# Kernel optimization log

Hardware: AMD Instinct MI355X
Metric: run time of the kernel (lower is better)

## Reference

```python
import jax, jax.numpy as jnp
import numpy as np

C = 512
GROUPS = 32
EPS = 1e-6


def setup_inputs() -> dict:
    key = jax.random.key(0)
    ks = jax.random.split(key, 10)
    s = 0.02
    return {
        "x": jax.random.normal(ks[0], (2, C, 64, 64), dtype=jnp.float32),
        "gn_scale": jnp.ones((C,), jnp.float32),
        "gn_bias": jnp.zeros((C,), jnp.float32),
        "wq": jax.random.normal(ks[1], (C, C), jnp.float32) * s,
        "bq": jnp.zeros((C,), jnp.float32),
        "wk": jax.random.normal(ks[2], (C, C), jnp.float32) * s,
        "bk": jnp.zeros((C,), jnp.float32),
        "wv": jax.random.normal(ks[3], (C, C), jnp.float32) * s,
        "bv": jnp.zeros((C,), jnp.float32),
        "wo": jax.random.normal(ks[4], (C, C), jnp.float32) * s,
        "bo": jnp.zeros((C,), jnp.float32),
    }


def group_norm(x, scale, bias):
    # x: [b, c, h, w]; 32 groups over channel dim
    b, c, h, w = x.shape
    xg = x.reshape(b, GROUPS, c // GROUPS, h, w)
    mean = jnp.mean(xg, axis=(2, 3, 4), keepdims=True)
    var = jnp.var(xg, axis=(2, 3, 4), keepdims=True)
    xg = (xg - mean) * jax.lax.rsqrt(var + EPS)
    x = xg.reshape(b, c, h, w)
    return x * scale[None, :, None, None] + bias[None, :, None, None]


def reference(x, gn_scale, gn_bias, wq, bq, wk, bk, wv, bv, wo, bo):
    b, c, h, w = x.shape
    n = h * w
    hn = group_norm(x, gn_scale, gn_bias).reshape(b, c, n)  # [b,c,n]
    # 1x1 conv == channel matmul: out[b,o,n] = W[o,i] @ h[b,i,n] + bias
    q = jnp.einsum('oi,bin->bon', wq, hn) + bq[None, :, None]
    k = jnp.einsum('oi,bin->bon', wk, hn) + bk[None, :, None]
    v = jnp.einsum('oi,bin->bon', wv, hn) + bv[None, :, None]
    # weight[b, i, j] = q_i . k_j, softmax over j
    scale = int(c) ** (-0.5)
    weight = jnp.einsum('bci,bcj->bij', q, k) * scale  # [b,n,n]
    weight = jax.nn.softmax(weight, axis=2)
    # h[b,c,i] = sum_j v[b,c,j] * weight[b,i,j]
    out = jnp.einsum('bcj,bij->bci', v, weight)
    out = jnp.einsum('oi,bin->bon', wo, out) + bo[None, :, None]
    return out.reshape(b, c, h, w) + x
```

## Files before the change

### kernel.cpp

```cpp
#include <hip/hip_runtime.h>
#include <hip/hip_bf16.h>


typedef __attribute__((ext_vector_type(8))) short short8_t;
typedef __attribute__((ext_vector_type(4))) short short4_t;
typedef __attribute__((ext_vector_type(4))) float f32x4;

__device__ __forceinline__ void gload16(const void* g, void* l) {
  __builtin_amdgcn_global_load_lds(
      (const __attribute__((address_space(1))) void*)g,
      (__attribute__((address_space(3))) void*)l, 16, 0, 0);
}

__device__ __forceinline__ short f2bf_bits(float f) {
  __hip_bfloat16 h = __float2bfloat16(f);
  return *reinterpret_cast<short*>(&h);
}
__device__ __forceinline__ float bfbits2f(short s) {
  union { unsigned int u; float f; } c;
  c.u = ((unsigned int)(unsigned short)s) << 16;
  return c.f;
}

__global__ __launch_bounds__(512)
void s_gemm8(const __hip_bfloat16* __restrict__ qk,
             __hip_bfloat16* __restrict__ P, float c)
{
  const long long QKz = 4096LL * 1024;
  const long long SS  = 4096LL * 4096;

  const int b = blockIdx.x;
  const int bz = b >> 8;
  const int r = b & 255, xcd = r & 7, sl = r >> 3;
  const int bm = (xcd >> 1) * 4 + (sl & 3);
  const int bn = (xcd & 1) * 8 + (sl >> 2);

  const __hip_bfloat16* Aq = qk + (size_t)bz * QKz;
  const __hip_bfloat16* Bk = Aq + 512;

  const int tid = threadIdx.x;
  const int wid = tid >> 6, l = tid & 63;
  const int wrM = wid >> 2, wcN = wid & 3;
  const int lhi = l >> 4, llo = l & 15;

  __shared__ char sm[2 * 65536];

  f32x4 acc[2][2][4][2] = {};
  short8_t af[4][2], bf[2][2];

  const int rIn = l >> 3;
  const int colSw = 8 * ((l & 7) ^ (rIn & 7));
  const __hip_bfloat16* gA = Aq + (size_t)(bm * 256 + rIn) * 1024 + colSw;
  const __hip_bfloat16* gB = Bk + (size_t)(bn * 256 + rIn) * 1024 + colSw;

  auto STG = [&](int mat, int half, int t) {
    const __hip_bfloat16* src = mat ? gB : gA;
    char* dst = sm + (t & 1) * 65536 + mat * 32768;
    const int rb = half * 128 + wid * 16;
    gload16(src + (size_t)rb * 1024 + t * 64, dst + rb * 128);
    gload16(src + (size_t)(rb + 8) * 1024 + t * 64, dst + (rb + 8) * 128);
  };

#define PHASE(MH, NH, RBUF, WAITN, LA, LB, ...) do {                          \
    asm volatile("s_waitcnt vmcnt(" #WAITN ")" ::: "memory");                 \
    __builtin_amdgcn_sched_barrier(0);                                        \
    const char* bbA = sm + (RBUF) * 65536;                                    \
    const char* bbB = bbA + 32768;                                            \
    if (LA) {                                                                 \
      _Pragma("unroll") for (int m = 0; m < 4; ++m) {                         \
        const int rowA = (MH) * 128 + wrM * 64 + m * 16 + llo;                \
        _Pragma("unroll") for (int kk = 0; kk < 2; ++kk)                      \
          af[m][kk] = *(const short8_t*)(bbA + rowA * 128 +                   \
                        (((kk * 4 + lhi) ^ (rowA & 7)) * 16));                \
      }                                                                       \
    }                                                                         \
    if (LB) {                                                                 \
      _Pragma("unroll") for (int n = 0; n < 2; ++n) {                         \
        const int rowB = (NH) * 128 + wcN * 32 + n * 16 + llo;                \
        _Pragma("unroll") for (int kk = 0; kk < 2; ++kk)                      \
          bf[n][kk] = *(const short8_t*)(bbB + rowB * 128 +                   \
                        (((kk * 4 + lhi) ^ (rowB & 7)) * 16));                \
      }                                                                       \
    }                                                                         \
    __VA_ARGS__;                                                              \
    __builtin_amdgcn_sched_barrier(0);                                        \
    __builtin_amdgcn_s_barrier();                                             \
    __builtin_amdgcn_sched_barrier(0);                                        \
    __builtin_amdgcn_s_setprio(1);                                            \
    _Pragma("unroll") for (int kk = 0; kk < 2; ++kk)                          \
      _Pragma("unroll") for (int m = 0; m < 4; ++m)                           \
        _Pragma("unroll") for (int n = 0; n < 2; ++n)                         \
          acc[MH][NH][m][n] = __builtin_amdgcn_mfma_f32_16x16x32_bf16(        \
              af[m][kk], bf[n][kk], acc[MH][NH][m][n], 0, 0, 0);              \
    __builtin_amdgcn_s_setprio(0);                                            \
    __builtin_amdgcn_sched_barrier(0);                                        \
    __builtin_amdgcn_s_barrier();                                             \
    __builtin_amdgcn_sched_barrier(0);                                        \
  } while (0)

  STG(0, 0, 0); STG(1, 0, 0); STG(0, 1, 0); STG(1, 1, 0);
  STG(0, 0, 1); STG(1, 0, 1); STG(0, 1, 1); STG(1, 1, 1);
  asm volatile("s_waitcnt vmcnt(0)" ::: "memory");
  __builtin_amdgcn_sched_barrier(0);
  __builtin_amdgcn_s_barrier();
  __builtin_amdgcn_sched_barrier(0);

  for (int i = 0; i < 3; ++i) {
    const int t1 = 2 * i + 1, t2 = 2 * i + 2, t3 = 2 * i + 3;
    PHASE(0, 0, 0, 4, 1, 1, if (i >= 1) STG(1, 0, t1));
    PHASE(0, 1, 0, 4, 0, 1, STG(0, 0, t2));
    PHASE(1, 1, 0, 4, 1, 0, STG(1, 1, t2));
    PHASE(1, 0, 0, 4, 0, 1, STG(0, 1, t2));
    PHASE(0, 0, 1, 4, 1, 1, STG(1, 0, t2));
    PHASE(0, 1, 1, 4, 0, 1, STG(0, 0, t3));
    PHASE(1, 1, 1, 4, 1, 0, STG(1, 1, t3));
    PHASE(1, 0, 1, 4, 0, 1, STG(0, 1, t3));
  }
  {
    PHASE(0, 0, 0, 0, 1, 1, STG(1, 0, 7));
    PHASE(0, 1, 0, 0, 0, 1, );
    PHASE(1, 1, 0, 0, 1, 0, );
    PHASE(1, 0, 0, 0, 0, 1, );
    PHASE(0, 0, 1, 0, 1, 1, );
    PHASE(0, 1, 1, 0, 0, 1, );
    PHASE(1, 1, 1, 0, 1, 0, );
    PHASE(1, 0, 1, 0, 0, 1, );
  }
#undef PHASE

  __hip_bfloat16* Pb = P + (size_t)bz * SS;
#pragma unroll
  for (int Mh = 0; Mh < 2; ++Mh)
#pragma unroll
    for (int m = 0; m < 4; ++m)
#pragma unroll
      for (int rr = 0; rr < 4; ++rr) {
        const int grow = bm * 256 + Mh * 128 + wrM * 64 + m * 16 + lhi * 4 + rr;
#pragma unroll
        for (int Nh = 0; Nh < 2; ++Nh)
#pragma unroll
          for (int n = 0; n < 2; ++n) {
            const int gcol = bn * 256 + Nh * 128 + wcN * 32 + n * 16 + llo;
            Pb[(size_t)grow * 4096 + gcol] =
                __float2bfloat16(exp2f(acc[Mh][Nh][m][n][rr] * c));
          }
      }
}

__global__ __launch_bounds__(256)
void rowsum_recip(const __hip_bfloat16* __restrict__ P, float* __restrict__ rs,
                  long long strZ)
{
  const int row = blockIdx.x, z = blockIdx.y;
  const __hip_bfloat16* p = P + (size_t)z * strZ + (size_t)row * 4096;
  const int tid = threadIdx.x;
  short8_t a = *(const short8_t*)(p + tid * 16);
  short8_t bq = *(const short8_t*)(p + tid * 16 + 8);
  float s = 0.f;
#pragma unroll
  for (int i = 0; i < 8; ++i) { s += bfbits2f(a[i]); s += bfbits2f(bq[i]); }
#pragma unroll
  for (int o = 32; o; o >>= 1) s += __shfl_xor(s, o);
  __shared__ float red[4];
  if ((tid & 63) == 0) red[tid >> 6] = s;
  __syncthreads();
  if (tid == 0) {
    s = red[0] + red[1] + red[2] + red[3];
    rs[(size_t)z * 4096 + row] = 1.f / s;
  }
}

template<int OUTF, int BIASMODE, int RESID, int PIPE, int SWZ, int MF, int NORM>
__global__ __launch_bounds__(256, 2)
void gemm_nt(const __hip_bfloat16* __restrict__ A,
             const __hip_bfloat16* __restrict__ B,
             void* __restrict__ Cv,
             const float* __restrict__ bias,
             const float* __restrict__ resid,
             const float* __restrict__ rnorm,
             float scale, int M, int N, int K,
             int lda, int ldb, int ldc,
             long long strA, long long strB, long long strC, long long strR)
{
  int bm, bn, bz;
  if (SWZ == 0) {
    bm = blockIdx.x; bn = blockIdx.y; bz = blockIdx.z;
  } else if (SWZ == 2) {
    const int b = blockIdx.x;
    bz = b >> 10;
    const int b2 = b & 1023;
    const int xcd = b2 & 7, s = b2 >> 3;
    bm = (xcd >> 1) * 8 + (s & 7);
    bn = (xcd & 1) * 16 + (s >> 3);
  } else {
    const int b = blockIdx.x;
    const int xcd = b & 7, slot = b >> 3;
    bm = slot & 7;
    const int panel = xcd * 8 + (slot >> 3);
    bn = panel & 31; bz = panel >> 5;
  }
  const int z = bz;
  A += (size_t)z * strA;
  B += (size_t)z * strB;

  const int tid = threadIdx.x;
  const int w = tid >> 6, l = tid & 63;
  const int wr = w >> 1, wc = w & 1;
  const int lhi = l >> 4, llo = l & 15;
  const int m0 = bm * (MF * 32), n0 = bn * 128;

  constexpr int BUFSZ = MF * 4096 + 16384;
  __shared__ char sm[(PIPE ? 2 : 1) * BUFSZ];

  f32x4 acc[MF][4] = {};

  const int rowInCh = l >> 3;
  const int colOff = 8 * ((l & 7) ^ (rowInCh & 7));

  const __hip_bfloat16* gAr[MF];
  const __hip_bfloat16* gBr[4];
#pragma unroll
  for (int j = 0; j < MF; ++j)
    gAr[j] = A + (size_t)(m0 + w * (8 * MF) + j * 8 + rowInCh) * lda + colOff;
#pragma unroll
  for (int r = 0; r < 4; ++r)
    gBr[r] = B + (size_t)(n0 + w * 32 + r * 8 + rowInCh) * ldb + colOff;

  auto stage = [&](int kt, int buf) {
    char* sA = sm + buf * BUFSZ;
    char* sB = sA + MF * 4096;
    const int ko = kt * 64;
#pragma unroll
    for (int j = 0; j < MF; ++j)
      gload16(gAr[j] + ko, sA + (w * MF + j) * 1024);
#pragma unroll
    for (int r = 0; r < 4; ++r)
      gload16(gBr[r] + ko, sB + (w * 4 + r) * 1024);
  };

  auto compute = [&](int buf) {
    char* sA = sm + buf * BUFSZ;
    char* sB = sA + MF * 4096;
#pragma unroll
    for (int kk = 0; kk < 2; ++kk) {
      short8_t af[MF], bfv[4];
#pragma unroll
      for (int m = 0; m < MF; ++m) {
        const int row = wr * (16 * MF) + m * 16 + llo;
        const int inner = ((kk * 4 + lhi) ^ (row & 7)) * 16;
        af[m] = *(const short8_t*)(sA + row * 128 + inner);
      }
#pragma unroll
      for (int n = 0; n < 4; ++n) {
        const int row = wc * 64 + n * 16 + llo;
        const int inner = ((kk * 4 + lhi) ^ (row & 7)) * 16;
        bfv[n] = *(const short8_t*)(sB + row * 128 + inner);
      }
#pragma unroll
      for (int m = 0; m < MF; ++m)
#pragma unroll
        for (int n = 0; n < 4; ++n)
          acc[m][n] = __builtin_amdgcn_mfma_f32_16x16x32_bf16(af[m], bfv[n], acc[m][n], 0, 0, 0);
    }
  };

  const int nkt = K >> 6;
  if (PIPE) {
    stage(0, 0);
    __syncthreads();
    int cur = 0;
    for (int kt = 0; kt < nkt; ++kt) {
      if (kt + 1 < nkt) stage(kt + 1, cur ^ 1);
      compute(cur);
      __syncthreads();
      cur ^= 1;
    }
  } else {
    for (int kt = 0; kt < nkt; ++kt) {
      __syncthreads();
      stage(kt, 0);
      __syncthreads();
      compute(0);
    }
  }

#pragma unroll
  for (int m = 0; m < MF; ++m) {
#pragma unroll
    for (int r = 0; r < 4; ++r) {
      const int grow = m0 + wr * (16 * MF) + m * 16 + lhi * 4 + r;
#pragma unroll
      for (int n = 0; n < 4; ++n) {
        const int gcol = n0 + wc * 64 + n * 16 + llo;
        float v = acc[m][n][r] * scale;
        if (NORM) v *= rnorm[(size_t)z * 4096 + gcol];
        if (BIASMODE == 1) v += bias[grow];
        if (BIASMODE == 2) v += bias[gcol];
        const size_t idx = (size_t)z * strC + (size_t)grow * ldc + gcol;
        if (RESID) v += resid[(size_t)z * strR + (size_t)grow * ldc + gcol];
        if (OUTF == 0) ((__hip_bfloat16*)Cv)[idx] = __float2bfloat16(v);
        else           ((float*)Cv)[idx] = v;
      }
    }
  }
}

__global__ __launch_bounds__(256)
void gn_partial(const float* __restrict__ x, float* __restrict__ part)
{
  const int g = blockIdx.x, sl = blockIdx.y, z = blockIdx.z;
  const int tid = threadIdx.x;
  const float* xf = x + (size_t)z * 512 * 4096 + (size_t)g * 16 * 4096 + (size_t)sl * 4096;
  const float4* px = reinterpret_cast<const float4*>(xf);
  float s = 0.f, q = 0.f;
#pragma unroll
  for (int i = 0; i < 4; ++i) {
    float4 v = px[tid + i * 256];
    s += v.x + v.y + v.z + v.w;
    q += v.x * v.x + v.y * v.y + v.z * v.z + v.w * v.w;
  }
#pragma unroll
  for (int o = 32; o; o >>= 1) { s += __shfl_xor(s, o); q += __shfl_xor(q, o); }
  __shared__ float rs[4], rq[4];
  if ((tid & 63) == 0) { rs[tid >> 6] = s; rq[tid >> 6] = q; }
  __syncthreads();
  if (tid == 0) {
    s = rs[0] + rs[1] + rs[2] + rs[3];
    q = rq[0] + rq[1] + rq[2] + rq[3];
    part[(((size_t)z * 32 + g) * 16 + sl) * 2 + 0] = s;
    part[(((size_t)z * 32 + g) * 16 + sl) * 2 + 1] = q;
  }
}

__global__ __launch_bounds__(64)
void gn_finalize(const float* __restrict__ part, float* __restrict__ stats, int n)
{
  const int i = threadIdx.x;
  if (i >= n) return;
  float s = 0.f, q = 0.f;
#pragma unroll
  for (int sl = 0; sl < 16; ++sl) {
    s += part[(i * 16 + sl) * 2 + 0];
    q += part[(i * 16 + sl) * 2 + 1];
  }
  const float mean = s * (1.0f / 65536.0f);
  const float var = q * (1.0f / 65536.0f) - mean * mean;
  stats[i * 2 + 0] = mean;
  stats[i * 2 + 1] = rsqrtf(var + 1e-6f);
}

__global__ __launch_bounds__(256)
void gn_apply_t(const float* __restrict__ x, const float* __restrict__ stats,
                const float* __restrict__ gns, const float* __restrict__ gnb,
                __hip_bfloat16* __restrict__ ht)
{
  const int st = blockIdx.x, ct = blockIdx.y, z = blockIdx.z;
  const int tid = threadIdx.x;
  __shared__ float tile[64][65];
  const float* xb = x + (size_t)z * 512 * 4096;
  const int lane64 = tid & 63, rr = tid >> 6;
#pragma unroll
  for (int pp = 0; pp < 16; ++pp) {
    const int cl = pp * 4 + rr;
    const int c = ct * 64 + cl;
    const int g = c >> 4;
    const float mean = stats[(z * 32 + g) * 2 + 0];
    const float rstd = stats[(z * 32 + g) * 2 + 1];
    const float val = xb[(size_t)c * 4096 + st * 64 + lane64];
    tile[cl][lane64] = (val - mean) * rstd * gns[c] + gnb[c];
  }
  __syncthreads();
  __hip_bfloat16* hb = ht + (size_t)z * 4096 * 512;
#pragma unroll
  for (int pp = 0; pp < 16; ++pp) {
    const int sl = pp * 4 + rr;
    const int s = st * 64 + sl;
    hb[(size_t)s * 512 + ct * 64 + lane64] = __float2bfloat16(tile[lane64][sl]);
  }
}

__global__ __launch_bounds__(256)
void softmax_rows(__hip_bfloat16* __restrict__ S, long long strZ)
{
  const int row = blockIdx.x, z = blockIdx.y;
  __hip_bfloat16* p = S + (size_t)z * strZ + (size_t)row * 4096;
  const int tid = threadIdx.x;
  short8_t a = *(const short8_t*)(p + tid * 16);
  short8_t b = *(const short8_t*)(p + tid * 16 + 8);
  float v[16];
#pragma unroll
  for (int i = 0; i < 8; ++i) { v[i] = bfbits2f(a[i]); v[8 + i] = bfbits2f(b[i]); }
  float m = v[0];
#pragma unroll
  for (int i = 1; i < 16; ++i) m = fmaxf(m, v[i]);
#pragma unroll
  for (int o = 32; o; o >>= 1) m = fmaxf(m, __shfl_xor(m, o));
  __shared__ float red[8];
  if ((tid & 63) == 0) red[tid >> 6] = m;
  __syncthreads();
  m = fmaxf(fmaxf(red[0], red[1]), fmaxf(red[2], red[3]));
  float s = 0.f;
#pragma unroll
  for (int i = 0; i < 16; ++i) { v[i] = exp2f((v[i] - m) * 1.44269504f); s += v[i]; }
#pragma unroll
  for (int o = 32; o; o >>= 1) s += __shfl_xor(s, o);
  __syncthreads();
  if ((tid & 63) == 0) red[4 + (tid >> 6)] = s;
  __syncthreads();
  s = red[4] + red[5] + red[6] + red[7];
  const float inv = 1.f / s;
#pragma unroll
  for (int i = 0; i < 8; ++i) { a[i] = f2bf_bits(v[i] * inv); b[i] = f2bf_bits(v[8 + i] * inv); }
  *(short8_t*)(p + tid * 16) = a;
  *(short8_t*)(p + tid * 16 + 8) = b;
}

__global__ __launch_bounds__(256)
void cast3(const float* __restrict__ w0, const float* __restrict__ w1,
           const float* __restrict__ w2, __hip_bfloat16* __restrict__ out)
{
  const int j = blockIdx.y;
  const float* src = (j == 0) ? w0 : (j == 1) ? w1 : w2;
  const int i = blockIdx.x * 256 + threadIdx.x;
  float4 v = reinterpret_cast<const float4*>(src)[i];
  short4_t o;
  o[0] = f2bf_bits(v.x); o[1] = f2bf_bits(v.y);
  o[2] = f2bf_bits(v.z); o[3] = f2bf_bits(v.w);
  *reinterpret_cast<short4_t*>((short*)out + (size_t)j * 262144 + (size_t)i * 4) = o;
}

__global__ __launch_bounds__(256)
void transpose_cast(const float* __restrict__ w, __hip_bfloat16* __restrict__ wt)
{
  __shared__ float tile[64][65];
  const int ct = blockIdx.x, it = blockIdx.y;
  const int tid = threadIdx.x;
  const int lane = tid & 63, rr = tid >> 6;
#pragma unroll
  for (int p = 0; p < 16; ++p) {
    const int cl = p * 4 + rr;
    tile[cl][lane] = w[(size_t)(ct * 64 + cl) * 512 + it * 64 + lane];
  }
  __syncthreads();
#pragma unroll
  for (int p = 0; p < 16; ++p) {
    const int il = p * 4 + rr;
    wt[(size_t)(it * 64 + il) * 512 + ct * 64 + lane] = __float2bfloat16(tile[lane][il]);
  }
}

__global__ __launch_bounds__(64)
void prep_bias(const float* __restrict__ wo, const float* __restrict__ bv,
               const float* __restrict__ bo, const float* __restrict__ bq,
               const float* __restrict__ bk,
               float* __restrict__ bvo, float* __restrict__ bqk)
{
  const int o = blockIdx.x * 64 + threadIdx.x;
  const float4* row = reinterpret_cast<const float4*>(wo + (size_t)o * 512);
  const float4* b4 = reinterpret_cast<const float4*>(bv);
  float s = 0.f;
#pragma unroll 8
  for (int i = 0; i < 128; ++i) {
    float4 a = row[i], b = b4[i];
    s += a.x * b.x + a.y * b.y + a.z * b.z + a.w * b.w;
  }
  bvo[o] = s + bo[o];
  bqk[o] = bq[o];
  bqk[512 + o] = bk[o];
}

extern "C" void kernel_launch(void* const* d_in, const int* in_sizes, int n_in,
                              void* d_out, int out_size, void* d_ws, size_t ws_size,
                              hipStream_t stream)
{
  const float* x   = (const float*)d_in[0];
  const float* gns = (const float*)d_in[1];
  const float* gnb = (const float*)d_in[2];
  const float* wq  = (const float*)d_in[3];
  const float* bq  = (const float*)d_in[4];
  const float* wk  = (const float*)d_in[5];
  const float* bk  = (const float*)d_in[6];
  const float* wv  = (const float*)d_in[7];
  const float* bv  = (const float*)d_in[8];
  const float* wo  = (const float*)d_in[9];
  const float* bo  = (const float*)d_in[10];
  float* out = (float*)d_out;

  const int WB = 512 * 512;
  const long long HT  = 4096LL * 512;
  const long long QKz = 4096LL * 1024;
  const long long VOz = 512LL * 4096;
  const long long SS  = 4096LL * 4096;
  const long long CHW = 512LL * 4096;

  char* base = (char*)d_ws;
  size_t off = 0;
  auto alloc = [&](size_t b) { void* r = base + off; off = (off + b + 255) & ~(size_t)255; return r; };

  __hip_bfloat16* wbf = (__hip_bfloat16*)alloc((size_t)5 * WB * 2);
  float* bqk   = (float*)alloc(1024 * 4);
  float* bvo   = (float*)alloc(512 * 4);
  float* part  = (float*)alloc(2 * 32 * 16 * 2 * 4);
  float* stats = (float*)alloc(2 * 32 * 2 * 4);
  float* rsum  = (float*)alloc(2 * 4096 * 4);
  const size_t fixed = off;

  const size_t qkB = (size_t)2 * QKz * 2;
  const size_t voB = (size_t)2 * VOz * 2;
  const size_t sB2 = (size_t)2 * SS * 2;
  const size_t sB1 = (size_t)SS * 2;
  const int MODE = (ws_size >= fixed + qkB + voB + sB2) ? 2 : 1;

  __hip_bfloat16* qk   = (__hip_bfloat16*)alloc(qkB);
  __hip_bfloat16* vo   = (__hip_bfloat16*)alloc(voB);
  const size_t sbufB = (MODE == 2) ? sB2 : sB1;
  __hip_bfloat16* sbuf = (__hip_bfloat16*)alloc(sbufB);
  __hip_bfloat16* ht = (__hip_bfloat16*)((char*)sbuf + sbufB - (size_t)2 * HT * 2);

  __hip_bfloat16* wqk = wbf;
  __hip_bfloat16* woB = wbf + 2 * WB;
  __hip_bfloat16* wvT = wbf + 3 * WB;
  __hip_bfloat16* wvo = wbf + 4 * WB;

  const float SC = 0.04419417382415922f;
  const float CEXP = SC * 1.4426950408889634f;

  cast3<<<dim3(256, 3), 256, 0, stream>>>(wq, wk, wo, wbf);
  transpose_cast<<<dim3(8, 8), 256, 0, stream>>>(wv, wvT);
  prep_bias<<<8, 64, 0, stream>>>(wo, bv, bo, bq, bk, bvo, bqk);
  gn_partial<<<dim3(32, 16, 2), 256, 0, stream>>>(x, part);
  gn_finalize<<<1, 64, 0, stream>>>(part, stats, 64);

  gemm_nt<0, 0, 0, 1, 0, 4, 0><<<dim3(4, 4, 1), 256, 0, stream>>>(
      woB, wvT, wvo, nullptr, nullptr, nullptr, 1.f, 512, 512, 512,
      512, 512, 512, 0, 0, 0, 0);

  gn_apply_t<<<dim3(64, 8, 2), 256, 0, stream>>>(x, stats, gns, gnb, ht);

  gemm_nt<0, 2, 0, 1, 0, 4, 0><<<dim3(32, 8, 2), 256, 0, stream>>>(
      ht, wqk, qk, bqk, nullptr, nullptr, 1.f, 4096, 1024, 512,
      512, 512, 1024, HT, 0, QKz, 0);

  gemm_nt<0, 0, 0, 1, 3, 2, 0><<<dim3(512, 1, 1), 256, 0, stream>>>(
      wvo, ht, vo, nullptr, nullptr, nullptr, 1.f, 512, 4096, 512,
      512, 512, 4096, 0, HT, VOz, 0);

  if (MODE == 2) {
    s_gemm8<<<512, 512, 0, stream>>>(qk, sbuf, CEXP);
    rowsum_recip<<<dim3(4096, 2), 256, 0, stream>>>(sbuf, rsum, SS);
    gemm_nt<1, 1, 1, 1, 3, 2, 1><<<dim3(512, 1, 1), 256, 0, stream>>>(
        vo, sbuf, out, bvo, x, rsum, 1.f, 512, 4096, 4096,
        4096, 4096, 4096, VOz, SS, CHW, CHW);
  } else {
    for (int z = 0; z < 2; ++z) {
      gemm_nt<0, 0, 0, 0, 0, 4, 0><<<dim3(32, 32, 1), 256, 0, stream>>>(
          qk + (size_t)z * QKz, qk + (size_t)z * QKz + 512, sbuf, nullptr, nullptr,
          nullptr, SC, 4096, 4096, 512, 1024, 1024, 4096, 0, 0, 0, 0);
      softmax_rows<<<dim3(4096, 1), 256, 0, stream>>>(sbuf, 0);
      gemm_nt<1, 1, 1, 1, 0, 2, 0><<<dim3(8, 32, 1), 256, 0, stream>>>(
          vo + (size_t)z * VOz, sbuf, out + (size_t)z * CHW, bvo, x + (size_t)z * CHW,
          nullptr, 1.f, 512, 4096, 4096, 4096, 4096, 4096, 0, 0, 0, 0);
    }
  }
}
```

Measured before the change: 159.5 us.

## Fuse softmax row-sum into score GEMM epilogue and batch barriers per buffer

```diff
diff --git a/kernel.cpp b/kernel.cpp
--- a/kernel.cpp
+++ b/kernel.cpp
@@ -24,7 +24,8 @@
 
 __global__ __launch_bounds__(512)
 void s_gemm8(const __hip_bfloat16* __restrict__ qk,
-             __hip_bfloat16* __restrict__ P, float c)
+             __hip_bfloat16* __restrict__ P, float* __restrict__ part2,
+             float c)
 {
   const long long QKz = 4096LL * 1024;
   const long long SS  = 4096LL * 4096;
@@ -61,9 +62,14 @@
     gload16(src + (size_t)(rb + 8) * 1024 + t * 64, dst + (rb + 8) * 128);
   };
 
-#define PHASE(MH, NH, RBUF, WAITN, LA, LB, ...) do {                          \
-    asm volatile("s_waitcnt vmcnt(" #WAITN ")" ::: "memory");                 \
+#define GSTART(N) do {                                                        \
+    asm volatile("s_waitcnt vmcnt(" #N ")" ::: "memory");                     \
     __builtin_amdgcn_sched_barrier(0);                                        \
+    __builtin_amdgcn_s_barrier();                                             \
+    __builtin_amdgcn_sched_barrier(0);                                        \
+  } while (0)
+
+#define PHASE(MH, NH, RBUF, LA, LB, ...) do {                                 \
     const char* bbA = sm + (RBUF) * 65536;                                    \
     const char* bbB = bbA + 32768;                                            \
     if (LA) {                                                                 \
@@ -107,28 +113,34 @@
 
   for (int i = 0; i < 3; ++i) {
     const int t1 = 2 * i + 1, t2 = 2 * i + 2, t3 = 2 * i + 3;
-    PHASE(0, 0, 0, 4, 1, 1, if (i >= 1) STG(1, 0, t1));
-    PHASE(0, 1, 0, 4, 0, 1, STG(0, 0, t2));
-    PHASE(1, 1, 0, 4, 1, 0, STG(1, 1, t2));
-    PHASE(1, 0, 0, 4, 0, 1, STG(0, 1, t2));
-    PHASE(0, 0, 1, 4, 1, 1, STG(1, 0, t2));
-    PHASE(0, 1, 1, 4, 0, 1, STG(0, 0, t3));
-    PHASE(1, 1, 1, 4, 1, 0, STG(1, 1, t3));
-    PHASE(1, 0, 1, 4, 0, 1, STG(0, 1, t3));
+    GSTART(6);
+    PHASE(0, 0, 0, 1, 1, if (i >= 1) STG(1, 0, t1));
+    PHASE(0, 1, 0, 0, 1, STG(0, 0, t2));
+    PHASE(1, 1, 0, 1, 0, STG(1, 1, t2));
+    PHASE(1, 0, 0, 0, 1, STG(0, 1, t2));
+    GSTART(6);
+    PHASE(0, 0, 1, 1, 1, STG(1, 0, t2));
+    PHASE(0, 1, 1, 0, 1, STG(0, 0, t3));
+    PHASE(1, 1, 1, 1, 0, STG(1, 1, t3));
+    PHASE(1, 0, 1, 0, 1, STG(0, 1, t3));
   }
   {
-    PHASE(0, 0, 0, 0, 1, 1, STG(1, 0, 7));
-    PHASE(0, 1, 0, 0, 0, 1, );
-    PHASE(1, 1, 0, 0, 1, 0, );
-    PHASE(1, 0, 0, 0, 0, 1, );
-    PHASE(0, 0, 1, 0, 1, 1, );
-    PHASE(0, 1, 1, 0, 0, 1, );
-    PHASE(1, 1, 1, 0, 1, 0, );
-    PHASE(1, 0, 1, 0, 0, 1, );
+    GSTART(6);
+    PHASE(0, 0, 0, 1, 1, STG(1, 0, 7));
+    PHASE(0, 1, 0, 0, 1, );
+    PHASE(1, 1, 0, 1, 0, );
+    PHASE(1, 0, 0, 0, 1, );
+    GSTART(0);
+    PHASE(0, 0, 1, 1, 1, );
+    PHASE(0, 1, 1, 0, 1, );
+    PHASE(1, 1, 1, 1, 0, );
+    PHASE(1, 0, 1, 0, 1, );
   }
 #undef PHASE
+#undef GSTART
 
   __hip_bfloat16* Pb = P + (size_t)bz * SS;
+  float rp[2][4][4];
 #pragma unroll
   for (int Mh = 0; Mh < 2; ++Mh)
 #pragma unroll
@@ -136,38 +148,59 @@
 #pragma unroll
       for (int rr = 0; rr < 4; ++rr) {
         const int grow = bm * 256 + Mh * 128 + wrM * 64 + m * 16 + lhi * 4 + rr;
+        float s = 0.f;
 #pragma unroll
         for (int Nh = 0; Nh < 2; ++Nh)
 #pragma unroll
           for (int n = 0; n < 2; ++n) {
             const int gcol = bn * 256 + Nh * 128 + wcN * 32 + n * 16 + llo;
-            Pb[(size_t)grow * 4096 + gcol] =
-                __float2bfloat16(exp2f(acc[Mh][Nh][m][n][rr] * c));
+            const float v = exp2f(acc[Mh][Nh][m][n][rr] * c);
+            Pb[(size_t)grow * 4096 + gcol] = __float2bfloat16(v);
+            s += v;
           }
+        rp[Mh][m][rr] = s;
       }
+#pragma unroll
+  for (int Mh = 0; Mh < 2; ++Mh)
+#pragma unroll
+    for (int m = 0; m < 4; ++m)
+#pragma unroll
+      for (int rr = 0; rr < 4; ++rr) {
+        float s = rp[Mh][m][rr];
+        s += __shfl_xor(s, 1); s += __shfl_xor(s, 2);
+        s += __shfl_xor(s, 4); s += __shfl_xor(s, 8);
+        rp[Mh][m][rr] = s;
+      }
+  __syncthreads();
+  float* rsl = (float*)sm;
+  if (llo == 0) {
+#pragma unroll
+    for (int Mh = 0; Mh < 2; ++Mh)
+#pragma unroll
+      for (int m = 0; m < 4; ++m)
+#pragma unroll
+        for (int rr = 0; rr < 4; ++rr) {
+          const int rl = Mh * 128 + wrM * 64 + m * 16 + lhi * 4 + rr;
+          rsl[rl * 4 + wcN] = rp[Mh][m][rr];
+        }
+  }
+  __syncthreads();
+  if (tid < 256) {
+    const float s = rsl[tid * 4] + rsl[tid * 4 + 1] + rsl[tid * 4 + 2] + rsl[tid * 4 + 3];
+    part2[((size_t)bz * 16 + bn) * 4096 + bm * 256 + tid] = s;
+  }
 }
 
 __global__ __launch_bounds__(256)
-void rowsum_recip(const __hip_bfloat16* __restrict__ P, float* __restrict__ rs,
-                  long long strZ)
-{
-  const int row = blockIdx.x, z = blockIdx.y;
-  const __hip_bfloat16* p = P + (size_t)z * strZ + (size_t)row * 4096;
-  const int tid = threadIdx.x;
-  short8_t a = *(const short8_t*)(p + tid * 16);
-  short8_t bq = *(const short8_t*)(p + tid * 16 + 8);
+void rs_final(const float* __restrict__ part2, float* __restrict__ rs)
+{
+  const int i = blockIdx.x * 256 + threadIdx.x;
+  const int z = i >> 12, row = i & 4095;
   float s = 0.f;
 #pragma unroll
-  for (int i = 0; i < 8; ++i) { s += bfbits2f(a[i]); s += bfbits2f(bq[i]); }
-#pragma unroll
-  for (int o = 32; o; o >>= 1) s += __shfl_xor(s, o);
-  __shared__ float red[4];
-  if ((tid & 63) == 0) red[tid >> 6] = s;
-  __syncthreads();
-  if (tid == 0) {
-    s = red[0] + red[1] + red[2] + red[3];
-    rs[(size_t)z * 4096 + row] = 1.f / s;
-  }
+  for (int bn = 0; bn < 16; ++bn)
+    s += part2[((size_t)z * 16 + bn) * 4096 + row];
+  rs[(size_t)z * 4096 + row] = 1.f / s;
 }
 
 template<int OUTF, int BIASMODE, int RESID, int PIPE, int SWZ, int MF, int NORM>
@@ -503,6 +536,7 @@
   float* part  = (float*)alloc(2 * 32 * 16 * 2 * 4);
   float* stats = (float*)alloc(2 * 32 * 2 * 4);
   float* rsum  = (float*)alloc(2 * 4096 * 4);
+  float* part2 = (float*)alloc((size_t)2 * 16 * 4096 * 4);
   const size_t fixed = off;
 
   const size_t qkB = (size_t)2 * QKz * 2;
@@ -546,8 +580,8 @@
       512, 512, 4096, 0, HT, VOz, 0);
 
   if (MODE == 2) {
-    s_gemm8<<<512, 512, 0, stream>>>(qk, sbuf, CEXP);
-    rowsum_recip<<<dim3(4096, 2), 256, 0, stream>>>(sbuf, rsum, SS);
+    s_gemm8<<<512, 512, 0, stream>>>(qk, sbuf, part2, CEXP);
+    rs_final<<<32, 256, 0, stream>>>(part2, rsum);
     gemm_nt<1, 1, 1, 1, 3, 2, 1><<<dim3(512, 1, 1), 256, 0, stream>>>(
         vo, sbuf, out, bvo, x, rsum, 1.f, 512, 4096, 4096,
         4096, 4096, 4096, VOz, SS, CHW, CHW);
```

Result: faster. 156.0 us (-2.2%).
